# Kernel optimization log

Hardware: AMD Instinct MI355X
Metric: run time of the kernel (lower is better)

## Reference

```python
import jax, jax.numpy as jnp
import numpy as np

N_NODES = 100000


def _gcn_layer(x, src, dst, deg_inv_sqrt, W, b):
    # GCNConv: out = D^{-1/2} (A + I) D^{-1/2} X W + b  (symmetric norm, self-loops)
    xw = x @ W  # [N, out]
    norm = deg_inv_sqrt[src] * deg_inv_sqrt[dst]  # [E]
    msg = xw[src] * norm[:, None]  # [E, out] gathered messages
    agg = jax.ops.segment_sum(msg, dst, num_segments=N_NODES)
    # self-loop contribution: norm_ii = deg_inv_sqrt[i]^2
    agg = agg + (deg_inv_sqrt * deg_inv_sqrt)[:, None] * xw
    return agg + b


def setup_inputs() -> dict:
    key = jax.random.key(0)
    k1, k2, k3, k4, k5, k6 = jax.random.split(key, 6)
    F_IN, HID, OUT, E = 128, 256, 40, 1600000
    x = jax.random.normal(k1, (N_NODES, F_IN), dtype=jnp.float32)
    edge_index = jax.random.randint(k2, (2, E), 0, N_NODES, dtype=jnp.int64)
    s1 = 1.0 / np.sqrt(F_IN)
    s2 = 1.0 / np.sqrt(HID)
    W1 = jax.random.uniform(k3, (F_IN, HID), jnp.float32, -s1, s1)
    b1 = jnp.zeros((HID,), jnp.float32)
    W2 = jax.random.uniform(k4, (HID, OUT), jnp.float32, -s2, s2)
    b2 = jnp.zeros((OUT,), jnp.float32)
    return {"x": x, "edge_index": edge_index, "W1": W1, "b1": b1, "W2": W2, "b2": b2}


def reference(x, edge_index, W1, b1, W2, b2):
    src, dst = edge_index[0], edge_index[1]
    # degree with self-loops (GCNConv default add_self_loops=True)
    deg = jax.ops.segment_sum(jnp.ones_like(dst, dtype=x.dtype), dst, num_segments=N_NODES) + 1.0
    deg_inv_sqrt = jax.lax.rsqrt(deg)
    h = _gcn_layer(x, src, dst, deg_inv_sqrt, W1, b1)
    h = jax.nn.relu(h)
    # dropout is identity in eval mode
    h = _gcn_layer(h, src, dst, deg_inv_sqrt, W2, b2)
    return jax.nn.log_softmax(h, axis=1)
```

## Files before the change

kernel.cpp:

```cpp
#include <hip/hip_runtime.h>
#include <math.h>

typedef long long ll;
typedef unsigned int uint;
typedef __attribute__((ext_vector_type(8))) short bf16x8;
typedef __attribute__((ext_vector_type(4))) float f32x4;

#define FIN 128
#define HID 256
#define FOUT 40
#define NG 8
#define NBIN 64
#define CAPPAD 65536
#define PERMBLKS 32

__device__ __forceinline__ float bflo(uint u) { return __uint_as_float(u << 16); }
__device__ __forceinline__ float bfhi(uint u) { return __uint_as_float(u & 0xFFFF0000u); }
__device__ __forceinline__ unsigned short f2bf(float f) {
  uint u = __float_as_uint(f);
  u += 0x7FFFu + ((u >> 16) & 1u);
  return (unsigned short)(u >> 16);
}

__device__ __forceinline__ int detect64(const uint* __restrict__ ei) {
  return (ei[1] == 0u && ei[3] == 0u && ei[5] == 0u && ei[7] == 0u) ? 1 : 0;
}

__global__ __launch_bounds__(256) void k_init(
    const void* __restrict__ ei,
    const float* __restrict__ W1, const float* __restrict__ W2,
    unsigned short* __restrict__ w1p, unsigned short* __restrict__ w2p,
    int2* __restrict__ partbuf, int* __restrict__ pcur,
    ll E, int range, ll cap) {
  __shared__ int wrun[4][NG], wbase[4][NG], lbase[NG];
  int t = threadIdx.x;
  int i = blockIdx.x * 256 + t;
  int lane = t & 63, w = t >> 6;

  if (i < 32768) {
    int j = i & 7, g = (i >> 3) & 3, c = (i >> 5) & 255, s = i >> 13;
    int k = s * 32 + g * 8 + j;
    w1p[i] = f2bf(W1[(size_t)k * HID + c]);
  } else if (i < 32768 + 12288) {
    int i2 = i - 32768;
    int j = i2 & 7, g = (i2 >> 3) & 3, q = i2 >> 5;
    int c = q % 48, s = q / 48;
    int k = s * 32 + g * 8 + j;
    w2p[i2] = (c < FOUT) ? f2bf(W2[(size_t)k * FOUT + c]) : (unsigned short)0;
  }

  int is64 = detect64((const uint*)ei);
  ll base = (ll)i * 4;
  int m = 0;
  int s[4], d[4], p[4] = {-1, -1, -1, -1};
  if (base < E) {
    m = (int)((E - base < 4) ? (E - base) : 4);
    if (is64) {
      if (m == 4) {
        longlong2 a0 = *(const longlong2*)((const ll*)ei + base);
        longlong2 a1 = *(const longlong2*)((const ll*)ei + base + 2);
        longlong2 b0 = *(const longlong2*)((const ll*)ei + E + base);
        longlong2 b1 = *(const longlong2*)((const ll*)ei + E + base + 2);
        s[0]=(int)a0.x; s[1]=(int)a0.y; s[2]=(int)a1.x; s[3]=(int)a1.y;
        d[0]=(int)b0.x; d[1]=(int)b0.y; d[2]=(int)b1.x; d[3]=(int)b1.y;
      } else {
        for (int j = 0; j < m; ++j) { s[j]=(int)((const ll*)ei)[base+j]; d[j]=(int)((const ll*)ei)[E+base+j]; }
      }
    } else {
      if (m == 4) {
        int4 a = *(const int4*)((const int*)ei + base);
        int4 b = *(const int4*)((const int*)ei + E + base);
        s[0]=a.x; s[1]=a.y; s[2]=a.z; s[3]=a.w;
        d[0]=b.x; d[1]=b.y; d[2]=b.z; d[3]=b.w;
      } else {
        for (int j = 0; j < m; ++j) { s[j]=((const int*)ei)[base+j]; d[j]=((const int*)ei)[E+base+j]; }
      }
    }
    for (int j = 0; j < m; ++j) p[j] = d[j] / range;
  }

  int run[NG] = {0,0,0,0,0,0,0,0};
  int rank[4] = {0,0,0,0};
  unsigned long long lt = (1ull << lane) - 1ull;
  #pragma unroll
  for (int j = 0; j < 4; ++j) {
    #pragma unroll
    for (int g = 0; g < NG; ++g) {
      unsigned long long mm = __ballot(p[j] == g);
      if (p[j] == g) rank[j] = run[g] + (int)__popcll(mm & lt);
      run[g] += (int)__popcll(mm);
    }
  }
  if (lane < NG) wrun[w][lane] = run[lane];
  __syncthreads();
  if (t < NG) {
    int acc = 0;
    for (int ww = 0; ww < 4; ++ww) { wbase[ww][t] = acc; acc += wrun[ww][t]; }
    lbase[t] = acc ? atomicAdd(&pcur[t], acc) : 0;
  }
  __syncthreads();
  for (int j = 0; j < m; ++j) {
    int g = p[j];
    ll slot = (ll)lbase[g] + wbase[w][g] + rank[j];
    if (slot < cap) partbuf[(ll)g * cap + slot] = make_int2(s[j], d[j]);
  }
}

__global__ __launch_bounds__(256) void k_count(
    const int2* __restrict__ partbuf, const int* __restrict__ pcur,
    int* __restrict__ cnt, ll cap) {
  int g = blockIdx.x & (NG - 1);
  const int2* pb = partbuf + (ll)g * cap;
  int cnt_g = min(pcur[g], (int)cap);
  int bg = blockIdx.x >> 3, NB = gridDim.x >> 3;
  for (int i = bg * 256 + threadIdx.x; i < cnt_g; i += NB * 256) {
    int2 p = pb[i];
    atomicAdd(&cnt[p.y], 1);
  }
}

__global__ __launch_bounds__(1024) void k_scan1(const int* __restrict__ cnt,
                                                int* __restrict__ row_off,
                                                int* __restrict__ blksums, int n) {
  __shared__ int sm[1024];
  int t = threadIdx.x;
  int base = blockIdx.x * 4096 + t * 4;
  int v0 = (base + 0 < n) ? cnt[base + 0] : 0;
  int v1 = (base + 1 < n) ? cnt[base + 1] : 0;
  int v2 = (base + 2 < n) ? cnt[base + 2] : 0;
  int v3 = (base + 3 < n) ? cnt[base + 3] : 0;
  int s = v0 + v1 + v2 + v3;
  sm[t] = s;
  __syncthreads();
  for (int off = 1; off < 1024; off <<= 1) {
    int u = (t >= off) ? sm[t - off] : 0;
    __syncthreads();
    sm[t] += u;
    __syncthreads();
  }
  int excl = sm[t] - s;
  if (base + 0 < n) row_off[base + 0] = excl;
  if (base + 1 < n) row_off[base + 1] = excl + v0;
  if (base + 2 < n) row_off[base + 2] = excl + v0 + v1;
  if (base + 3 < n) row_off[base + 3] = excl + v0 + v1 + v2;
  if (t == 1023) blksums[blockIdx.x] = s ? sm[1023] : sm[1023];
}

__global__ __launch_bounds__(1024) void k_scan3(
    int* __restrict__ row_off, int* __restrict__ cursor,
    const int* __restrict__ blksums, float* __restrict__ dis,
    int* __restrict__ hist, int n, int nb) {
  __shared__ int lh[NBIN];
  __shared__ int bpfx[256];
  int t = threadIdx.x;
  if (t < NBIN) lh[t] = 0;
  if (t == 0) {
    int acc = 0;
    for (int b = 0; b < nb; ++b) { bpfx[b] = acc; acc += blksums[b]; }
    bpfx[nb] = acc;
  }
  __syncthreads();
  int i = blockIdx.x * 1024 + t;
  if (i < n) {
    int c = cursor[i];
    int v = row_off[i] + bpfx[i >> 12];
    row_off[i] = v;
    cursor[i] = v;
    dis[i] = rsqrtf((float)c + 1.0f);
    atomicAdd(&lh[min(c, NBIN - 1)], 1);
  }
  if (i == 0) row_off[n] = bpfx[nb];
  __syncthreads();
  if (t < NBIN && lh[t]) atomicAdd(&hist[t], lh[t]);
}

__global__ __launch_bounds__(256) void k_fillperm(
    const int2* __restrict__ partbuf, const int* __restrict__ pcur,
    int* __restrict__ cursor, int* __restrict__ csr, ll cap,
    const int* __restrict__ row_off, const int* __restrict__ hist,
    int* __restrict__ pbincur, int* __restrict__ perm, int n) {
  int t = threadIdx.x;
  if (blockIdx.x < PERMBLKS) {
    __shared__ int lh[NBIN], lbase[NBIN], pfx[NBIN];
    if (t < NBIN) { lh[t] = 0; pfx[t] = hist[t]; }
    __syncthreads();
    if (t == 0) {
      int acc = 0;
      for (int b = 0; b < NBIN; ++b) { int v = pfx[b]; pfx[b] = acc; acc += v; }
    }
    int base = blockIdx.x * 4096 + t * 16;
    int deg[16];
    #pragma unroll
    for (int j = 0; j < 16; ++j) {
      int i = base + j;
      if (i < n) {
        deg[j] = min(row_off[i + 1] - row_off[i], NBIN - 1);
        atomicAdd(&lh[deg[j]], 1);
      } else deg[j] = -1;
    }
    __syncthreads();
    if (t < NBIN) {
      lbase[t] = pfx[t] + (lh[t] ? atomicAdd(&pbincur[t], lh[t]) : 0);
      lh[t] = 0;
    }
    __syncthreads();
    #pragma unroll
    for (int j = 0; j < 16; ++j) {
      if (deg[j] >= 0) {
        int r = atomicAdd(&lh[deg[j]], 1);
        perm[lbase[deg[j]] + r] = base + j;
      }
    }
  } else {
    int bid = blockIdx.x - PERMBLKS;
    int g = blockIdx.x & (NG - 1);
    const int2* pb = partbuf + (ll)g * cap;
    int cnt_g = min(pcur[g], (int)cap);
    int bg = bid >> 3, NB = (gridDim.x - PERMBLKS) >> 3;
    for (int i = bg * 256 + t; i < cnt_g; i += NB * 256) {
      int2 p = pb[i];
      int pos = atomicAdd(&cursor[p.y], 1);
      csr[pos] = p.x;
    }
  }
}

__global__ __launch_bounds__(256) void k_xcast(
    const float* __restrict__ x, const float* __restrict__ dis,
    unsigned short* __restrict__ xb, int total8) {
  int i = blockIdx.x * 256 + threadIdx.x;
  if (i >= total8) return;
  float w = dis[i >> 4];
  const float4* p = (const float4*)x + (size_t)i * 2;
  float4 a = p[0], b = p[1];
  uint4 o;
  o.x = (uint)f2bf(w * a.x) | ((uint)f2bf(w * a.y) << 16);
  o.y = (uint)f2bf(w * a.z) | ((uint)f2bf(w * a.w) << 16);
  o.z = (uint)f2bf(w * b.x) | ((uint)f2bf(w * b.y) << 16);
  o.w = (uint)f2bf(w * b.z) | ((uint)f2bf(w * b.w) << 16);
  *(uint4*)(xb + (size_t)i * 8) = o;
}

__device__ __forceinline__ void add8(float* a, uint4 r) {
  a[0] += bflo(r.x); a[1] += bfhi(r.x);
  a[2] += bflo(r.y); a[3] += bfhi(r.y);
  a[4] += bflo(r.z); a[5] += bfhi(r.z);
  a[6] += bflo(r.w); a[7] += bfhi(r.w);
}

__global__ __launch_bounds__(256) void k_fused1(
    const unsigned short* __restrict__ xb, const int* __restrict__ csr,
    const int* __restrict__ row_off, const float* __restrict__ dis,
    const int* __restrict__ perm,
    const unsigned short* __restrict__ w1p, const float* __restrict__ b1,
    const unsigned short* __restrict__ w2p, unsigned short* __restrict__ xw2b,
    int n, int ntiles, int stride)
{
  __shared__ __align__(16) unsigned short xsb[16 * 136];
  __shared__ __align__(16) unsigned short hsb[16 * 264];
  __shared__ int   nid[16];
  __shared__ float dsh[16];

  int tid = threadIdx.x;
  int tile = (int)(((ll)blockIdx.x * stride) % ntiles);
  int n0 = tile * 16;
  int wv = tid >> 6, lane = tid & 63, qq = lane >> 4, l16 = lane & 15;
  int nl = wv * 4 + qq;
  int idx = n0 + nl;
  int node = (idx < n) ? perm[idx] : -1;

  float a[8] = {0, 0, 0, 0, 0, 0, 0, 0};
  float di = 0.f;
  if (node >= 0) {
    di = dis[node];
    uint4 v = *((const uint4*)(xb + (size_t)node * FIN) + l16);
    add8(a, v);
    int e0 = row_off[node], e1 = row_off[node + 1];
    int e = e0;
    for (; e + 8 <= e1; e += 8) {
      int s0 = csr[e],     s1 = csr[e + 1], s2 = csr[e + 2], s3 = csr[e + 3];
      int s4 = csr[e + 4], s5 = csr[e + 5], s6 = csr[e + 6], s7 = csr[e + 7];
      uint4 r0 = *((const uint4*)(xb + (size_t)s0 * FIN) + l16);
      uint4 r1 = *((const uint4*)(xb + (size_t)s1 * FIN) + l16);
      uint4 r2 = *((const uint4*)(xb + (size_t)s2 * FIN) + l16);
      uint4 r3 = *((const uint4*)(xb + (size_t)s3 * FIN) + l16);
      uint4 r4 = *((const uint4*)(xb + (size_t)s4 * FIN) + l16);
      uint4 r5 = *((const uint4*)(xb + (size_t)s5 * FIN) + l16);
      uint4 r6 = *((const uint4*)(xb + (size_t)s6 * FIN) + l16);
      uint4 r7 = *((const uint4*)(xb + (size_t)s7 * FIN) + l16);
      add8(a, r0); add8(a, r1); add8(a, r2); add8(a, r3);
      add8(a, r4); add8(a, r5); add8(a, r6); add8(a, r7);
    }
    if (e < e1) {
      int last = e1 - 1;
      int s0 = csr[e];
      int s1 = csr[min(e + 1, last)], s2 = csr[min(e + 2, last)];
      int s3 = csr[min(e + 3, last)], s4 = csr[min(e + 4, last)];
      int s5 = csr[min(e + 5, last)], s6 = csr[min(e + 6, last)];
      int s7 = csr[min(e + 7, last)];
      uint4 r0 = *((const uint4*)(xb + (size_t)s0 * FIN) + l16);
      uint4 r1 = *((const uint4*)(xb + (size_t)s1 * FIN) + l16);
      uint4 r2 = *((const uint4*)(xb + (size_t)s2 * FIN) + l16);
      uint4 r3 = *((const uint4*)(xb + (size_t)s3 * FIN) + l16);
      uint4 r4 = *((const uint4*)(xb + (size_t)s4 * FIN) + l16);
      uint4 r5 = *((const uint4*)(xb + (size_t)s5 * FIN) + l16);
      uint4 r6 = *((const uint4*)(xb + (size_t)s6 * FIN) + l16);
      uint4 r7 = *((const uint4*)(xb + (size_t)s7 * FIN) + l16);
      uint4 z = make_uint4(0, 0, 0, 0);
      if (e + 1 > last) r1 = z;
      if (e + 2 > last) r2 = z;
      if (e + 3 > last) r3 = z;
      if (e + 4 > last) r4 = z;
      if (e + 5 > last) r5 = z;
      if (e + 6 > last) r6 = z;
      if (e + 7 > last) r7 = z;
      add8(a, r0); add8(a, r1); add8(a, r2); add8(a, r3);
      add8(a, r4); add8(a, r5); add8(a, r6); add8(a, r7);
    }
  }
  if (l16 == 0) { nid[nl] = node; dsh[nl] = di; }
  {
    uint4 pk;
    pk.x = (uint)f2bf(di * a[0]) | ((uint)f2bf(di * a[1]) << 16);
    pk.y = (uint)f2bf(di * a[2]) | ((uint)f2bf(di * a[3]) << 16);
    pk.z = (uint)f2bf(di * a[4]) | ((uint)f2bf(di * a[5]) << 16);
    pk.w = (uint)f2bf(di * a[6]) | ((uint)f2bf(di * a[7]) << 16);
    *(uint4*)(xsb + nl * 136 + l16 * 8) = pk;
  }
  __syncthreads();

  int mrow = lane & 15, g = lane >> 4;
  f32x4 acc1[4] = {{0,0,0,0},{0,0,0,0},{0,0,0,0},{0,0,0,0}};
  #pragma unroll
  for (int s = 0; s < 4; ++s) {
    bf16x8 av = *(const bf16x8*)(xsb + mrow * 136 + s * 32 + g * 8);
    #pragma unroll
    for (int t = 0; t < 4; ++t) {
      int c = wv * 64 + t * 16 + mrow;
      bf16x8 bv = *(const bf16x8*)(w1p + (((size_t)(s * 256 + c) * 4 + g) << 3));
      acc1[t] = __builtin_amdgcn_mfma_f32_16x16x32_bf16(av, bv, acc1[t], 0, 0, 0);
    }
  }
  #pragma unroll
  for (int t = 0; t < 4; ++t) {
    int c = wv * 64 + t * 16 + mrow;
    float bb = b1[c];
    #pragma unroll
    for (int r = 0; r < 4; ++r) {
      float v = fmaxf(acc1[t][r] + bb, 0.f);
      hsb[(g * 4 + r) * 264 + c] = f2bf(v);
    }
  }
  __syncthreads();

  if (wv < 3) {
    f32x4 acc2 = {0, 0, 0, 0};
    int c2 = wv * 16 + mrow;
    #pragma unroll
    for (int s = 0; s < 8; ++s) {
      bf16x8 av = *(const bf16x8*)(hsb + mrow * 264 + s * 32 + g * 8);
      bf16x8 bv = *(const bf16x8*)(w2p + (((size_t)(s * 48 + c2) * 4 + g) << 3));
      acc2 = __builtin_amdgcn_mfma_f32_16x16x32_bf16(av, bv, acc2, 0, 0, 0);
    }
    if (c2 < FOUT) {
      #pragma unroll
      for (int r = 0; r < 4; ++r) {
        int nodeg = nid[g * 4 + r];
        if (nodeg >= 0)
          xw2b[(size_t)nodeg * FOUT + c2] = f2bf(acc2[r] * dsh[g * 4 + r]);
      }
    }
  }
}

__global__ __launch_bounds__(256) void k_layer2(
    const unsigned short* __restrict__ xw2b, const int* __restrict__ csr,
    const int* __restrict__ row_off, const float* __restrict__ dis,
    const int* __restrict__ perm,
    const float* __restrict__ b2, float* __restrict__ out,
    int n, int ntiles, int stride)
{
  int tid = threadIdx.x;
  int tile = (int)(((ll)blockIdx.x * stride) % ntiles);
  int idx = tile * 16 + (tid >> 4);
  int l16 = tid & 15;
  if (idx >= n) return;
  int node = perm[idx];
  float di = dis[node];
  bool act = (l16 < 10);
  float a0 = 0.f, a1 = 0.f, a2 = 0.f, a3 = 0.f;
  if (act) {
    uint2 v = *((const uint2*)(xw2b + (size_t)node * FOUT) + l16);
    a0 = bflo(v.x); a1 = bfhi(v.x); a2 = bflo(v.y); a3 = bfhi(v.y);
  }
  int e0 = row_off[node], e1 = row_off[node + 1];
  int e = e0;
  for (; e + 8 <= e1; e += 8) {
    int s0 = csr[e],     s1 = csr[e + 1], s2 = csr[e + 2], s3 = csr[e + 3];
    int s4 = csr[e + 4], s5 = csr[e + 5], s6 = csr[e + 6], s7 = csr[e + 7];
    if (act) {
      uint2 r0 = *((const uint2*)(xw2b + (size_t)s0 * FOUT) + l16);
      uint2 r1 = *((const uint2*)(xw2b + (size_t)s1 * FOUT) + l16);
      uint2 r2 = *((const uint2*)(xw2b + (size_t)s2 * FOUT) + l16);
      uint2 r3 = *((const uint2*)(xw2b + (size_t)s3 * FOUT) + l16);
      uint2 r4 = *((const uint2*)(xw2b + (size_t)s4 * FOUT) + l16);
      uint2 r5 = *((const uint2*)(xw2b + (size_t)s5 * FOUT) + l16);
      uint2 r6 = *((const uint2*)(xw2b + (size_t)s6 * FOUT) + l16);
      uint2 r7 = *((const uint2*)(xw2b + (size_t)s7 * FOUT) + l16);
      a0 += bflo(r0.x); a1 += bfhi(r0.x); a2 += bflo(r0.y); a3 += bfhi(r0.y);
      a0 += bflo(r1.x); a1 += bfhi(r1.x); a2 += bflo(r1.y); a3 += bfhi(r1.y);
      a0 += bflo(r2.x); a1 += bfhi(r2.x); a2 += bflo(r2.y); a3 += bfhi(r2.y);
      a0 += bflo(r3.x); a1 += bfhi(r3.x); a2 += bflo(r3.y); a3 += bfhi(r3.y);
      a0 += bflo(r4.x); a1 += bfhi(r4.x); a2 += bflo(r4.y); a3 += bfhi(r4.y);
      a0 += bflo(r5.x); a1 += bfhi(r5.x); a2 += bflo(r5.y); a3 += bfhi(r5.y);
      a0 += bflo(r6.x); a1 += bfhi(r6.x); a2 += bflo(r6.y); a3 += bfhi(r6.y);
      a0 += bflo(r7.x); a1 += bfhi(r7.x); a2 += bflo(r7.y); a3 += bfhi(r7.y);
    }
  }
  if (e < e1) {
    int last = e1 - 1;
    int s0 = csr[e];
    int s1 = csr[min(e + 1, last)], s2 = csr[min(e + 2, last)];
    int s3 = csr[min(e + 3, last)], s4 = csr[min(e + 4, last)];
    int s5 = csr[min(e + 5, last)], s6 = csr[min(e + 6, last)];
    int s7 = csr[min(e + 7, last)];
    if (act) {
      uint2 z = make_uint2(0, 0);
      uint2 r0 = *((const uint2*)(xw2b + (size_t)s0 * FOUT) + l16);
      uint2 r1 = *((const uint2*)(xw2b + (size_t)s1 * FOUT) + l16);
      uint2 r2 = *((const uint2*)(xw2b + (size_t)s2 * FOUT) + l16);
      uint2 r3 = *((const uint2*)(xw2b + (size_t)s3 * FOUT) + l16);
      uint2 r4 = *((const uint2*)(xw2b + (size_t)s4 * FOUT) + l16);
      uint2 r5 = *((const uint2*)(xw2b + (size_t)s5 * FOUT) + l16);
      uint2 r6 = *((const uint2*)(xw2b + (size_t)s6 * FOUT) + l16);
      uint2 r7 = *((const uint2*)(xw2b + (size_t)s7 * FOUT) + l16);
      if (e + 1 > last) r1 = z;
      if (e + 2 > last) r2 = z;
      if (e + 3 > last) r3 = z;
      if (e + 4 > last) r4 = z;
      if (e + 5 > last) r5 = z;
      if (e + 6 > last) r6 = z;
      if (e + 7 > last) r7 = z;
      a0 += bflo(r0.x); a1 += bfhi(r0.x); a2 += bflo(r0.y); a3 += bfhi(r0.y);
      a0 += bflo(r1.x); a1 += bfhi(r1.x); a2 += bflo(r1.y); a3 += bfhi(r1.y);
      a0 += bflo(r2.x); a1 += bfhi(r2.x); a2 += bflo(r2.y); a3 += bfhi(r2.y);
      a0 += bflo(r3.x); a1 += bfhi(r3.x); a2 += bflo(r3.y); a3 += bfhi(r3.y);
      a0 += bflo(r4.x); a1 += bfhi(r4.x); a2 += bflo(r4.y); a3 += bfhi(r4.y);
      a0 += bflo(r5.x); a1 += bfhi(r5.x); a2 += bflo(r5.y); a3 += bfhi(r5.y);
      a0 += bflo(r6.x); a1 += bfhi(r6.x); a2 += bflo(r6.y); a3 += bfhi(r6.y);
      a0 += bflo(r7.x); a1 += bfhi(r7.x); a2 += bflo(r7.y); a3 += bfhi(r7.y);
    }
  }
  float l0 = -INFINITY, l1 = -INFINITY, l2 = -INFINITY, l3 = -INFINITY;
  if (act) {
    float4 bv = *(const float4*)(b2 + l16 * 4);
    l0 = di * a0 + bv.x; l1 = di * a1 + bv.y;
    l2 = di * a2 + bv.z; l3 = di * a3 + bv.w;
  }
  float m = fmaxf(fmaxf(l0, l1), fmaxf(l2, l3));
  #pragma unroll
  for (int off = 8; off > 0; off >>= 1) m = fmaxf(m, __shfl_xor(m, off));
  float s = 0.f;
  if (act) s = expf(l0 - m) + expf(l1 - m) + expf(l2 - m) + expf(l3 - m);
  #pragma unroll
  for (int off = 8; off > 0; off >>= 1) s += __shfl_xor(s, off);
  if (act) {
    float ls = m + logf(s);
    float4 o = make_float4(l0 - ls, l1 - ls, l2 - ls, l3 - ls);
    *(float4*)(out + (size_t)node * FOUT + l16 * 4) = o;
  }
}

extern "C" void kernel_launch(void* const* d_in, const int* in_sizes, int n_in,
                              void* d_out, int out_size, void* d_ws, size_t ws_size,
                              hipStream_t stream) {
  const float* x  = (const float*)d_in[0];
  const void*  ei = d_in[1];
  const float* W1 = (const float*)d_in[2];
  const float* b1 = (const float*)d_in[3];
  const float* W2 = (const float*)d_in[4];
  const float* b2 = (const float*)d_in[5];
  float* out = (float*)d_out;

  int n = in_sizes[0] / FIN;
  ll  E = (ll)in_sizes[1] / 2;
  int nb = (n + 4095) / 4096;
  int range = (n + NG - 1) / NG;
  ll  cap = E / NG + CAPPAD;

  int ntiles = (n + 15) / 16;
  int stride = 1;
  for (int c = (ntiles * 2 / 5) | 1; c < ntiles; c += 2) {
    int a = c, b = ntiles;
    while (b) { int r = a % b; a = b; b = r; }
    if (a == 1) { stride = c; break; }
  }

  char* ws = (char*)d_ws;
  size_t off = 0;
  auto carve = [&](size_t bytes) -> char* {
    char* p = ws + off;
    off = (off + bytes + 255) & ~(size_t)255;
    return p;
  };
  int zn = n + NBIN + NBIN + NG;
  int*   zbase   = (int*)carve((size_t)zn * 4);
  int*   cursor  = zbase;
  int*   hist    = zbase + n;
  int*   pbincur = zbase + n + NBIN;
  int*   pcur    = zbase + n + NBIN + NBIN;
  int*   row_off = (int*)carve((size_t)(n + 1) * 4);
  int2*  partbuf = (int2*)carve((size_t)NG * cap * 8);
  int*   csr     = (int*)carve((size_t)E * 4);
  int*   blksums = (int*)carve(256 * 4);
  int*   perm    = (int*)carve((size_t)n * 4);
  float* dis     = (float*)carve((size_t)n * 4);
  unsigned short* xb   = (unsigned short*)carve((size_t)n * FIN * 2);
  unsigned short* w1p  = (unsigned short*)carve(32768 * 2);
  unsigned short* w2p  = (unsigned short*)carve(12288 * 2);
  unsigned short* xw2b = (unsigned short*)carve((size_t)n * FOUT * 2);
  (void)n_in; (void)out_size; (void)ws_size;

  int gx8   = (n * FIN / 8 + 255) / 256;
  int ginit = (int)((E + 1023) / 1024);

  hipMemsetAsync(zbase, 0, (size_t)zn * 4, stream);

  hipLaunchKernelGGL(k_init,  dim3(ginit), dim3(256), 0, stream,
                     ei, W1, W2, w1p, w2p, partbuf, pcur, E, range, cap);
  hipLaunchKernelGGL(k_count, dim3(2048), dim3(256), 0, stream, partbuf, pcur, cursor, cap);
  hipLaunchKernelGGL(k_scan1, dim3(nb), dim3(1024), 0, stream, cursor, row_off, blksums, n);
  hipLaunchKernelGGL(k_scan3, dim3((n + 1023) / 1024), dim3(1024), 0, stream,
                     row_off, cursor, blksums, dis, hist, n, nb);
  hipLaunchKernelGGL(k_fillperm, dim3(2048 + PERMBLKS), dim3(256), 0, stream,
                     partbuf, pcur, cursor, csr, cap, row_off, hist, pbincur, perm, n);
  hipLaunchKernelGGL(k_xcast, dim3(gx8), dim3(256), 0, stream, x, dis, xb, n * FIN / 8);
  hipLaunchKernelGGL(k_fused1, dim3(ntiles), dim3(256), 0, stream,
                     xb, csr, row_off, dis, perm, w1p, b1, w2p, xw2b, n, ntiles, stride);
  hipLaunchKernelGGL(k_layer2, dim3(ntiles), dim3(256), 0, stream,
                     xw2b, csr, row_off, dis, perm, b2, out, n, ntiles, stride);
}
```

Measured before the change: 296.1 us.

## Fuse xcast into fillperm, process 4 tiles per block, widen layer2 gather

Folds the x-to-bf16 cast kernel into the fillperm launch as extra blocks, removing one kernel launch and letting the cast run alongside the CSR fill. Both aggregation kernels now loop over four 16-node tiles per block, cutting the grid size and amortizing block setup, with the stride permutation recomputed over groups. Layer 2's gather is rewritten to batch 16 clamped neighbor loads with predicated accumulation. The trade-off is fewer blocks available to hide gather latency and extra barriers per iteration.

```diff
diff --git a/kernel.cpp b/kernel.cpp
--- a/kernel.cpp
+++ b/kernel.cpp
@@ -13,6 +13,8 @@
 #define NBIN 64
 #define CAPPAD 65536
 #define PERMBLKS 32
+#define FILLBLKS 2048
+#define TPB1 4
 
 __device__ __forceinline__ float bflo(uint u) { return __uint_as_float(u << 16); }
 __device__ __forceinline__ float bfhi(uint u) { return __uint_as_float(u & 0xFFFF0000u); }
@@ -143,7 +145,7 @@
   if (base + 1 < n) row_off[base + 1] = excl + v0;
   if (base + 2 < n) row_off[base + 2] = excl + v0 + v1;
   if (base + 3 < n) row_off[base + 3] = excl + v0 + v1 + v2;
-  if (t == 1023) blksums[blockIdx.x] = s ? sm[1023] : sm[1023];
+  if (t == 1023) blksums[blockIdx.x] = sm[1023];
 }
 
 __global__ __launch_bounds__(1024) void k_scan3(
@@ -178,7 +180,9 @@
     const int2* __restrict__ partbuf, const int* __restrict__ pcur,
     int* __restrict__ cursor, int* __restrict__ csr, ll cap,
     const int* __restrict__ row_off, const int* __restrict__ hist,
-    int* __restrict__ pbincur, int* __restrict__ perm, int n) {
+    int* __restrict__ pbincur, int* __restrict__ perm, int n,
+    const float* __restrict__ x, const float* __restrict__ dis,
+    unsigned short* __restrict__ xb, int total8) {
   int t = threadIdx.x;
   if (blockIdx.x < PERMBLKS) {
     __shared__ int lh[NBIN], lbase[NBIN], pfx[NBIN];
@@ -211,34 +215,30 @@
         perm[lbase[deg[j]] + r] = base + j;
       }
     }
-  } else {
+  } else if (blockIdx.x < PERMBLKS + FILLBLKS) {
     int bid = blockIdx.x - PERMBLKS;
     int g = blockIdx.x & (NG - 1);
     const int2* pb = partbuf + (ll)g * cap;
     int cnt_g = min(pcur[g], (int)cap);
-    int bg = bid >> 3, NB = (gridDim.x - PERMBLKS) >> 3;
+    int bg = bid >> 3, NB = FILLBLKS >> 3;
     for (int i = bg * 256 + t; i < cnt_g; i += NB * 256) {
       int2 p = pb[i];
       int pos = atomicAdd(&cursor[p.y], 1);
       csr[pos] = p.x;
     }
-  }
-}
-
-__global__ __launch_bounds__(256) void k_xcast(
-    const float* __restrict__ x, const float* __restrict__ dis,
-    unsigned short* __restrict__ xb, int total8) {
-  int i = blockIdx.x * 256 + threadIdx.x;
-  if (i >= total8) return;
-  float w = dis[i >> 4];
-  const float4* p = (const float4*)x + (size_t)i * 2;
-  float4 a = p[0], b = p[1];
-  uint4 o;
-  o.x = (uint)f2bf(w * a.x) | ((uint)f2bf(w * a.y) << 16);
-  o.y = (uint)f2bf(w * a.z) | ((uint)f2bf(w * a.w) << 16);
-  o.z = (uint)f2bf(w * b.x) | ((uint)f2bf(w * b.y) << 16);
-  o.w = (uint)f2bf(w * b.z) | ((uint)f2bf(w * b.w) << 16);
-  *(uint4*)(xb + (size_t)i * 8) = o;
+  } else {
+    int i = (blockIdx.x - PERMBLKS - FILLBLKS) * 256 + t;
+    if (i >= total8) return;
+    float w = dis[i >> 4];
+    const float4* p = (const float4*)x + (size_t)i * 2;
+    float4 a = p[0], b = p[1];
+    uint4 o;
+    o.x = (uint)f2bf(w * a.x) | ((uint)f2bf(w * a.y) << 16);
+    o.y = (uint)f2bf(w * a.z) | ((uint)f2bf(w * a.w) << 16);
+    o.z = (uint)f2bf(w * b.x) | ((uint)f2bf(w * b.y) << 16);
+    o.w = (uint)f2bf(w * b.z) | ((uint)f2bf(w * b.w) << 16);
+    *(uint4*)(xb + (size_t)i * 8) = o;
+  }
 }
 
 __device__ __forceinline__ void add8(float* a, uint4 r) {
@@ -254,7 +254,7 @@
     const int* __restrict__ perm,
     const unsigned short* __restrict__ w1p, const float* __restrict__ b1,
     const unsigned short* __restrict__ w2p, unsigned short* __restrict__ xw2b,
-    int n, int ntiles, int stride)
+    int n, int ngrp, int stride)
 {
   __shared__ __align__(16) unsigned short xsb[16 * 136];
   __shared__ __align__(16) unsigned short hsb[16 * 264];
@@ -262,114 +262,118 @@
   __shared__ float dsh[16];
 
   int tid = threadIdx.x;
-  int tile = (int)(((ll)blockIdx.x * stride) % ntiles);
-  int n0 = tile * 16;
+  int grp = (int)(((ll)blockIdx.x * stride) % ngrp);
   int wv = tid >> 6, lane = tid & 63, qq = lane >> 4, l16 = lane & 15;
   int nl = wv * 4 + qq;
-  int idx = n0 + nl;
-  int node = (idx < n) ? perm[idx] : -1;
-
-  float a[8] = {0, 0, 0, 0, 0, 0, 0, 0};
-  float di = 0.f;
-  if (node >= 0) {
-    di = dis[node];
-    uint4 v = *((const uint4*)(xb + (size_t)node * FIN) + l16);
-    add8(a, v);
-    int e0 = row_off[node], e1 = row_off[node + 1];
-    int e = e0;
-    for (; e + 8 <= e1; e += 8) {
-      int s0 = csr[e],     s1 = csr[e + 1], s2 = csr[e + 2], s3 = csr[e + 3];
-      int s4 = csr[e + 4], s5 = csr[e + 5], s6 = csr[e + 6], s7 = csr[e + 7];
-      uint4 r0 = *((const uint4*)(xb + (size_t)s0 * FIN) + l16);
-      uint4 r1 = *((const uint4*)(xb + (size_t)s1 * FIN) + l16);
-      uint4 r2 = *((const uint4*)(xb + (size_t)s2 * FIN) + l16);
-      uint4 r3 = *((const uint4*)(xb + (size_t)s3 * FIN) + l16);
-      uint4 r4 = *((const uint4*)(xb + (size_t)s4 * FIN) + l16);
-      uint4 r5 = *((const uint4*)(xb + (size_t)s5 * FIN) + l16);
-      uint4 r6 = *((const uint4*)(xb + (size_t)s6 * FIN) + l16);
-      uint4 r7 = *((const uint4*)(xb + (size_t)s7 * FIN) + l16);
-      add8(a, r0); add8(a, r1); add8(a, r2); add8(a, r3);
-      add8(a, r4); add8(a, r5); add8(a, r6); add8(a, r7);
-    }
-    if (e < e1) {
-      int last = e1 - 1;
-      int s0 = csr[e];
-      int s1 = csr[min(e + 1, last)], s2 = csr[min(e + 2, last)];
-      int s3 = csr[min(e + 3, last)], s4 = csr[min(e + 4, last)];
-      int s5 = csr[min(e + 5, last)], s6 = csr[min(e + 6, last)];
-      int s7 = csr[min(e + 7, last)];
-      uint4 r0 = *((const uint4*)(xb + (size_t)s0 * FIN) + l16);
-      uint4 r1 = *((const uint4*)(xb + (size_t)s1 * FIN) + l16);
-      uint4 r2 = *((const uint4*)(xb + (size_t)s2 * FIN) + l16);
-      uint4 r3 = *((const uint4*)(xb + (size_t)s3 * FIN) + l16);
-      uint4 r4 = *((const uint4*)(xb + (size_t)s4 * FIN) + l16);
-      uint4 r5 = *((const uint4*)(xb + (size_t)s5 * FIN) + l16);
-      uint4 r6 = *((const uint4*)(xb + (size_t)s6 * FIN) + l16);
-      uint4 r7 = *((const uint4*)(xb + (size_t)s7 * FIN) + l16);
-      uint4 z = make_uint4(0, 0, 0, 0);
-      if (e + 1 > last) r1 = z;
-      if (e + 2 > last) r2 = z;
-      if (e + 3 > last) r3 = z;
-      if (e + 4 > last) r4 = z;
-      if (e + 5 > last) r5 = z;
-      if (e + 6 > last) r6 = z;
-      if (e + 7 > last) r7 = z;
-      add8(a, r0); add8(a, r1); add8(a, r2); add8(a, r3);
-      add8(a, r4); add8(a, r5); add8(a, r6); add8(a, r7);
-    }
-  }
-  if (l16 == 0) { nid[nl] = node; dsh[nl] = di; }
-  {
-    uint4 pk;
-    pk.x = (uint)f2bf(di * a[0]) | ((uint)f2bf(di * a[1]) << 16);
-    pk.y = (uint)f2bf(di * a[2]) | ((uint)f2bf(di * a[3]) << 16);
-    pk.z = (uint)f2bf(di * a[4]) | ((uint)f2bf(di * a[5]) << 16);
-    pk.w = (uint)f2bf(di * a[6]) | ((uint)f2bf(di * a[7]) << 16);
-    *(uint4*)(xsb + nl * 136 + l16 * 8) = pk;
-  }
-  __syncthreads();
-
   int mrow = lane & 15, g = lane >> 4;
-  f32x4 acc1[4] = {{0,0,0,0},{0,0,0,0},{0,0,0,0},{0,0,0,0}};
-  #pragma unroll
-  for (int s = 0; s < 4; ++s) {
-    bf16x8 av = *(const bf16x8*)(xsb + mrow * 136 + s * 32 + g * 8);
-    #pragma unroll
-    for (int t = 0; t < 4; ++t) {
-      int c = wv * 64 + t * 16 + mrow;
-      bf16x8 bv = *(const bf16x8*)(w1p + (((size_t)(s * 256 + c) * 4 + g) << 3));
-      acc1[t] = __builtin_amdgcn_mfma_f32_16x16x32_bf16(av, bv, acc1[t], 0, 0, 0);
-    }
-  }
-  #pragma unroll
-  for (int t = 0; t < 4; ++t) {
-    int c = wv * 64 + t * 16 + mrow;
-    float bb = b1[c];
-    #pragma unroll
-    for (int r = 0; r < 4; ++r) {
-      float v = fmaxf(acc1[t][r] + bb, 0.f);
-      hsb[(g * 4 + r) * 264 + c] = f2bf(v);
-    }
-  }
-  __syncthreads();
-
-  if (wv < 3) {
-    f32x4 acc2 = {0, 0, 0, 0};
-    int c2 = wv * 16 + mrow;
-    #pragma unroll
-    for (int s = 0; s < 8; ++s) {
-      bf16x8 av = *(const bf16x8*)(hsb + mrow * 264 + s * 32 + g * 8);
-      bf16x8 bv = *(const bf16x8*)(w2p + (((size_t)(s * 48 + c2) * 4 + g) << 3));
-      acc2 = __builtin_amdgcn_mfma_f32_16x16x32_bf16(av, bv, acc2, 0, 0, 0);
-    }
-    if (c2 < FOUT) {
+
+  for (int tt = 0; tt < TPB1; ++tt) {
+    int n0 = (grp * TPB1 + tt) * 16;
+    int idx = n0 + nl;
+    int node = (idx < n) ? perm[idx] : -1;
+
+    float a[8] = {0, 0, 0, 0, 0, 0, 0, 0};
+    float di = 0.f;
+    if (node >= 0) {
+      di = dis[node];
+      uint4 v = *((const uint4*)(xb + (size_t)node * FIN) + l16);
+      add8(a, v);
+      int e0 = row_off[node], e1 = row_off[node + 1];
+      int e = e0;
+      for (; e + 8 <= e1; e += 8) {
+        int s0 = csr[e],     s1 = csr[e + 1], s2 = csr[e + 2], s3 = csr[e + 3];
+        int s4 = csr[e + 4], s5 = csr[e + 5], s6 = csr[e + 6], s7 = csr[e + 7];
+        uint4 r0 = *((const uint4*)(xb + (size_t)s0 * FIN) + l16);
+        uint4 r1 = *((const uint4*)(xb + (size_t)s1 * FIN) + l16);
+        uint4 r2 = *((const uint4*)(xb + (size_t)s2 * FIN) + l16);
+        uint4 r3 = *((const uint4*)(xb + (size_t)s3 * FIN) + l16);
+        uint4 r4 = *((const uint4*)(xb + (size_t)s4 * FIN) + l16);
+        uint4 r5 = *((const uint4*)(xb + (size_t)s5 * FIN) + l16);
+        uint4 r6 = *((const uint4*)(xb + (size_t)s6 * FIN) + l16);
+        uint4 r7 = *((const uint4*)(xb + (size_t)s7 * FIN) + l16);
+        add8(a, r0); add8(a, r1); add8(a, r2); add8(a, r3);
+        add8(a, r4); add8(a, r5); add8(a, r6); add8(a, r7);
+      }
+      if (e < e1) {
+        int last = e1 - 1;
+        int s0 = csr[e];
+        int s1 = csr[min(e + 1, last)], s2 = csr[min(e + 2, last)];
+        int s3 = csr[min(e + 3, last)], s4 = csr[min(e + 4, last)];
+        int s5 = csr[min(e + 5, last)], s6 = csr[min(e + 6, last)];
+        int s7 = csr[min(e + 7, last)];
+        uint4 r0 = *((const uint4*)(xb + (size_t)s0 * FIN) + l16);
+        uint4 r1 = *((const uint4*)(xb + (size_t)s1 * FIN) + l16);
+        uint4 r2 = *((const uint4*)(xb + (size_t)s2 * FIN) + l16);
+        uint4 r3 = *((const uint4*)(xb + (size_t)s3 * FIN) + l16);
+        uint4 r4 = *((const uint4*)(xb + (size_t)s4 * FIN) + l16);
+        uint4 r5 = *((const uint4*)(xb + (size_t)s5 * FIN) + l16);
+        uint4 r6 = *((const uint4*)(xb + (size_t)s6 * FIN) + l16);
+        uint4 r7 = *((const uint4*)(xb + (size_t)s7 * FIN) + l16);
+        uint4 z = make_uint4(0, 0, 0, 0);
+        if (e + 1 > last) r1 = z;
+        if (e + 2 > last) r2 = z;
+        if (e + 3 > last) r3 = z;
+        if (e + 4 > last) r4 = z;
+        if (e + 5 > last) r5 = z;
+        if (e + 6 > last) r6 = z;
+        if (e + 7 > last) r7 = z;
+        add8(a, r0); add8(a, r1); add8(a, r2); add8(a, r3);
+        add8(a, r4); add8(a, r5); add8(a, r6); add8(a, r7);
+      }
+    }
+    if (l16 == 0) { nid[nl] = node; dsh[nl] = di; }
+    {
+      uint4 pk;
+      pk.x = (uint)f2bf(di * a[0]) | ((uint)f2bf(di * a[1]) << 16);
+      pk.y = (uint)f2bf(di * a[2]) | ((uint)f2bf(di * a[3]) << 16);
+      pk.z = (uint)f2bf(di * a[4]) | ((uint)f2bf(di * a[5]) << 16);
+      pk.w = (uint)f2bf(di * a[6]) | ((uint)f2bf(di * a[7]) << 16);
+      *(uint4*)(xsb + nl * 136 + l16 * 8) = pk;
+    }
+    __syncthreads();
+
+    f32x4 acc1[4] = {{0,0,0,0},{0,0,0,0},{0,0,0,0},{0,0,0,0}};
+    #pragma unroll
+    for (int s = 0; s < 4; ++s) {
+      bf16x8 av = *(const bf16x8*)(xsb + mrow * 136 + s * 32 + g * 8);
+      #pragma unroll
+      for (int t2 = 0; t2 < 4; ++t2) {
+        int c = wv * 64 + t2 * 16 + mrow;
+        bf16x8 bv = *(const bf16x8*)(w1p + (((size_t)(s * 256 + c) * 4 + g) << 3));
+        acc1[t2] = __builtin_amdgcn_mfma_f32_16x16x32_bf16(av, bv, acc1[t2], 0, 0, 0);
+      }
+    }
+    #pragma unroll
+    for (int t2 = 0; t2 < 4; ++t2) {
+      int c = wv * 64 + t2 * 16 + mrow;
+      float bb = b1[c];
       #pragma unroll
       for (int r = 0; r < 4; ++r) {
-        int nodeg = nid[g * 4 + r];
-        if (nodeg >= 0)
-          xw2b[(size_t)nodeg * FOUT + c2] = f2bf(acc2[r] * dsh[g * 4 + r]);
-      }
-    }
+        float v = fmaxf(acc1[t2][r] + bb, 0.f);
+        hsb[(g * 4 + r) * 264 + c] = f2bf(v);
+      }
+    }
+    __syncthreads();
+
+    if (wv < 3) {
+      f32x4 acc2 = {0, 0, 0, 0};
+      int c2 = wv * 16 + mrow;
+      #pragma unroll
+      for (int s = 0; s < 8; ++s) {
+        bf16x8 av = *(const bf16x8*)(hsb + mrow * 264 + s * 32 + g * 8);
+        bf16x8 bv = *(const bf16x8*)(w2p + (((size_t)(s * 48 + c2) * 4 + g) << 3));
+        acc2 = __builtin_amdgcn_mfma_f32_16x16x32_bf16(av, bv, acc2, 0, 0, 0);
+      }
+      if (c2 < FOUT) {
+        #pragma unroll
+        for (int r = 0; r < 4; ++r) {
+          int nodeg = nid[g * 4 + r];
+          if (nodeg >= 0)
+            xw2b[(size_t)nodeg * FOUT + c2] = f2bf(acc2[r] * dsh[g * 4 + r]);
+        }
+      }
+    }
+    __syncthreads();
   }
 }
 
@@ -378,96 +382,61 @@
     const int* __restrict__ row_off, const float* __restrict__ dis,
     const int* __restrict__ perm,
     const float* __restrict__ b2, float* __restrict__ out,
-    int n, int ntiles, int stride)
+    int n, int ngrp, int stride)
 {
   int tid = threadIdx.x;
-  int tile = (int)(((ll)blockIdx.x * stride) % ntiles);
-  int idx = tile * 16 + (tid >> 4);
+  int grp = (int)(((ll)blockIdx.x * stride) % ngrp);
   int l16 = tid & 15;
-  if (idx >= n) return;
-  int node = perm[idx];
-  float di = dis[node];
   bool act = (l16 < 10);
-  float a0 = 0.f, a1 = 0.f, a2 = 0.f, a3 = 0.f;
-  if (act) {
-    uint2 v = *((const uint2*)(xw2b + (size_t)node * FOUT) + l16);
-    a0 = bflo(v.x); a1 = bfhi(v.x); a2 = bflo(v.y); a3 = bfhi(v.y);
-  }
-  int e0 = row_off[node], e1 = row_off[node + 1];
-  int e = e0;
-  for (; e + 8 <= e1; e += 8) {
-    int s0 = csr[e],     s1 = csr[e + 1], s2 = csr[e + 2], s3 = csr[e + 3];
-    int s4 = csr[e + 4], s5 = csr[e + 5], s6 = csr[e + 6], s7 = csr[e + 7];
+
+  for (int tt = 0; tt < TPB1; ++tt) {
+    int idx = (grp * TPB1 + tt) * 16 + (tid >> 4);
+    if (idx >= n) continue;
+    int node = perm[idx];
+    float di = dis[node];
+    float a0 = 0.f, a1 = 0.f, a2 = 0.f, a3 = 0.f;
     if (act) {
-      uint2 r0 = *((const uint2*)(xw2b + (size_t)s0 * FOUT) + l16);
-      uint2 r1 = *((const uint2*)(xw2b + (size_t)s1 * FOUT) + l16);
-      uint2 r2 = *((const uint2*)(xw2b + (size_t)s2 * FOUT) + l16);
-      uint2 r3 = *((const uint2*)(xw2b + (size_t)s3 * FOUT) + l16);
-      uint2 r4 = *((const uint2*)(xw2b + (size_t)s4 * FOUT) + l16);
-      uint2 r5 = *((const uint2*)(xw2b + (size_t)s5 * FOUT) + l16);
-      uint2 r6 = *((const uint2*)(xw2b + (size_t)s6 * FOUT) + l16);
-      uint2 r7 = *((const uint2*)(xw2b + (size_t)s7 * FOUT) + l16);
-      a0 += bflo(r0.x); a1 += bfhi(r0.x); a2 += bflo(r0.y); a3 += bfhi(r0.y);
-      a0 += bflo(r1.x); a1 += bfhi(r1.x); a2 += bflo(r1.y); a3 += bfhi(r1.y);
-      a0 += bflo(r2.x); a1 += bfhi(r2.x); a2 += bflo(r2.y); a3 += bfhi(r2.y);
-      a0 += bflo(r3.x); a1 += bfhi(r3.x); a2 += bflo(r3.y); a3 += bfhi(r3.y);
-      a0 += bflo(r4.x); a1 += bfhi(r4.x); a2 += bflo(r4.y); a3 += bfhi(r4.y);
-      a0 += bflo(r5.x); a1 += bfhi(r5.x); a2 += bflo(r5.y); a3 += bfhi(r5.y);
-      a0 += bflo(r6.x); a1 += bfhi(r6.x); a2 += bflo(r6.y); a3 += bfhi(r6.y);
-      a0 += bflo(r7.x); a1 += bfhi(r7.x); a2 += bflo(r7.y); a3 += bfhi(r7.y);
-    }
-  }
-  if (e < e1) {
-    int last = e1 - 1;
-    int s0 = csr[e];
-    int s1 = csr[min(e + 1, last)], s2 = csr[min(e + 2, last)];
-    int s3 = csr[min(e + 3, last)], s4 = csr[min(e + 4, last)];
-    int s5 = csr[min(e + 5, last)], s6 = csr[min(e + 6, last)];
-    int s7 = csr[min(e + 7, last)];
+      uint2 v = *((const uint2*)(xw2b + (size_t)node * FOUT) + l16);
+      a0 = bflo(v.x); a1 = bfhi(v.x); a2 = bflo(v.y); a3 = bfhi(v.y);
+    }
+    int e0 = row_off[node], e1 = row_off[node + 1];
+    for (int e = e0; e < e1; e += 16) {
+      int last = e1 - 1;
+      int sidx[16];
+      #pragma unroll
+      for (int j = 0; j < 16; ++j) sidx[j] = csr[min(e + j, last)];
+      if (act) {
+        uint2 r[16];
+        #pragma unroll
+        for (int j = 0; j < 16; ++j)
+          r[j] = *((const uint2*)(xw2b + (size_t)sidx[j] * FOUT) + l16);
+        #pragma unroll
+        for (int j = 0; j < 16; ++j) {
+          if (e + j <= last) {
+            a0 += bflo(r[j].x); a1 += bfhi(r[j].x);
+            a2 += bflo(r[j].y); a3 += bfhi(r[j].y);
+          }
+        }
+      }
+    }
+    float l0 = -INFINITY, l1 = -INFINITY, l2 = -INFINITY, l3 = -INFINITY;
     if (act) {
-      uint2 z = make_uint2(0, 0);
-      uint2 r0 = *((const uint2*)(xw2b + (size_t)s0 * FOUT) + l16);
-      uint2 r1 = *((const uint2*)(xw2b + (size_t)s1 * FOUT) + l16);
-      uint2 r2 = *((const uint2*)(xw2b + (size_t)s2 * FOUT) + l16);
-      uint2 r3 = *((const uint2*)(xw2b + (size_t)s3 * FOUT) + l16);
-      uint2 r4 = *((const uint2*)(xw2b + (size_t)s4 * FOUT) + l16);
-      uint2 r5 = *((const uint2*)(xw2b + (size_t)s5 * FOUT) + l16);
-      uint2 r6 = *((const uint2*)(xw2b + (size_t)s6 * FOUT) + l16);
-      uint2 r7 = *((const uint2*)(xw2b + (size_t)s7 * FOUT) + l16);
-      if (e + 1 > last) r1 = z;
-      if (e + 2 > last) r2 = z;
-      if (e + 3 > last) r3 = z;
-      if (e + 4 > last) r4 = z;
-      if (e + 5 > last) r5 = z;
-      if (e + 6 > last) r6 = z;
-      if (e + 7 > last) r7 = z;
-      a0 += bflo(r0.x); a1 += bfhi(r0.x); a2 += bflo(r0.y); a3 += bfhi(r0.y);
-      a0 += bflo(r1.x); a1 += bfhi(r1.x); a2 += bflo(r1.y); a3 += bfhi(r1.y);
-      a0 += bflo(r2.x); a1 += bfhi(r2.x); a2 += bflo(r2.y); a3 += bfhi(r2.y);
-      a0 += bflo(r3.x); a1 += bfhi(r3.x); a2 += bflo(r3.y); a3 += bfhi(r3.y);
-      a0 += bflo(r4.x); a1 += bfhi(r4.x); a2 += bflo(r4.y); a3 += bfhi(r4.y);
-      a0 += bflo(r5.x); a1 += bfhi(r5.x); a2 += bflo(r5.y); a3 += bfhi(r5.y);
-      a0 += bflo(r6.x); a1 += bfhi(r6.x); a2 += bflo(r6.y); a3 += bfhi(r6.y);
-      a0 += bflo(r7.x); a1 += bfhi(r7.x); a2 += bflo(r7.y); a3 += bfhi(r7.y);
-    }
-  }
-  float l0 = -INFINITY, l1 = -INFINITY, l2 = -INFINITY, l3 = -INFINITY;
-  if (act) {
-    float4 bv = *(const float4*)(b2 + l16 * 4);
-    l0 = di * a0 + bv.x; l1 = di * a1 + bv.y;
-    l2 = di * a2 + bv.z; l3 = di * a3 + bv.w;
-  }
-  float m = fmaxf(fmaxf(l0, l1), fmaxf(l2, l3));
-  #pragma unroll
-  for (int off = 8; off > 0; off >>= 1) m = fmaxf(m, __shfl_xor(m, off));
-  float s = 0.f;
-  if (act) s = expf(l0 - m) + expf(l1 - m) + expf(l2 - m) + expf(l3 - m);
-  #pragma unroll
-  for (int off = 8; off > 0; off >>= 1) s += __shfl_xor(s, off);
-  if (act) {
-    float ls = m + logf(s);
-    float4 o = make_float4(l0 - ls, l1 - ls, l2 - ls, l3 - ls);
-    *(float4*)(out + (size_t)node * FOUT + l16 * 4) = o;
+      float4 bv = *(const float4*)(b2 + l16 * 4);
+      l0 = di * a0 + bv.x; l1 = di * a1 + bv.y;
+      l2 = di * a2 + bv.z; l3 = di * a3 + bv.w;
+    }
+    float m = fmaxf(fmaxf(l0, l1), fmaxf(l2, l3));
+    #pragma unroll
+    for (int off = 8; off > 0; off >>= 1) m = fmaxf(m, __shfl_xor(m, off));
+    float s = 0.f;
+    if (act) s = expf(l0 - m) + expf(l1 - m) + expf(l2 - m) + expf(l3 - m);
+    #pragma unroll
+    for (int off = 8; off > 0; off >>= 1) s += __shfl_xor(s, off);
+    if (act) {
+      float ls = m + logf(s);
+      float4 o = make_float4(l0 - ls, l1 - ls, l2 - ls, l3 - ls);
+      *(float4*)(out + (size_t)node * FOUT + l16 * 4) = o;
+    }
   }
 }
 
@@ -489,9 +458,10 @@
   ll  cap = E / NG + CAPPAD;
 
   int ntiles = (n + 15) / 16;
+  int ngrp = (ntiles + TPB1 - 1) / TPB1;
   int stride = 1;
-  for (int c = (ntiles * 2 / 5) | 1; c < ntiles; c += 2) {
-    int a = c, b = ntiles;
+  for (int c = (ngrp * 2 / 5) | 1; c < ngrp; c += 2) {
+    int a = c, b = ngrp;
     while (b) { int r = a % b; a = b; b = r; }
     if (a == 1) { stride = c; break; }
   }
@@ -521,7 +491,8 @@
   unsigned short* xw2b = (unsigned short*)carve((size_t)n * FOUT * 2);
   (void)n_in; (void)out_size; (void)ws_size;
 
-  int gx8   = (n * FIN / 8 + 255) / 256;
+  int total8 = n * FIN / 8;
+  int gx8   = (total8 + 255) / 256;
   int ginit = (int)((E + 1023) / 1024);
 
   hipMemsetAsync(zbase, 0, (size_t)zn * 4, stream);
@@ -532,11 +503,11 @@
   hipLaunchKernelGGL(k_scan1, dim3(nb), dim3(1024), 0, stream, cursor, row_off, blksums, n);
   hipLaunchKernelGGL(k_scan3, dim3((n + 1023) / 1024), dim3(1024), 0, stream,
                      row_off, cursor, blksums, dis, hist, n, nb);
-  hipLaunchKernelGGL(k_fillperm, dim3(2048 + PERMBLKS), dim3(256), 0, stream,
-                     partbuf, pcur, cursor, csr, cap, row_off, hist, pbincur, perm, n);
-  hipLaunchKernelGGL(k_xcast, dim3(gx8), dim3(256), 0, stream, x, dis, xb, n * FIN / 8);
-  hipLaunchKernelGGL(k_fused1, dim3(ntiles), dim3(256), 0, stream,
-                     xb, csr, row_off, dis, perm, w1p, b1, w2p, xw2b, n, ntiles, stride);
-  hipLaunchKernelGGL(k_layer2, dim3(ntiles), dim3(256), 0, stream,
-                     xw2b, csr, row_off, dis, perm, b2, out, n, ntiles, stride);
-}
+  hipLaunchKernelGGL(k_fillperm, dim3(PERMBLKS + FILLBLKS + gx8), dim3(256), 0, stream,
+                     partbuf, pcur, cursor, csr, cap, row_off, hist, pbincur, perm, n,
+                     x, dis, xb, total8);
+  hipLaunchKernelGGL(k_fused1, dim3(ngrp), dim3(256), 0, stream,
+                     xb, csr, row_off, dis, perm, w1p, b1, w2p, xw2b, n, ngrp, stride);
+  hipLaunchKernelGGL(k_layer2, dim3(ngrp), dim3(256), 0, stream,
+                     xw2b, csr, row_off, dis, perm, b2, out, n, ngrp, stride);
+}
```

Measured after the change: 315.4 us. 1.07x slower.
